# Kernel optimization log

Hardware: AMD Instinct MI355X
Metric: run time of the kernel (lower is better)

The kernel has to match this reference:

```python
import jax, jax.numpy as jnp
import numpy as np

N_NODES = 50000
NEG_SLOPE = 0.2


def _gat_conv(x, src, dst, W, a_src, a_dst, b, num_nodes):
    # W: [H*C, F_in]; a_src/a_dst: [H, C]; b: [H*C]
    H, C = a_src.shape
    xp = (x @ W.T).reshape(num_nodes, H, C)              # [N,H,C]
    alpha_s = jnp.sum(xp * a_src[None], axis=-1)          # [N,H]
    alpha_d = jnp.sum(xp * a_dst[None], axis=-1)          # [N,H]
    e = jax.nn.leaky_relu(alpha_s[src] + alpha_d[dst], NEG_SLOPE)  # [E,H]
    # segment softmax over incoming edges of each dst node (self-loops guarantee non-empty segments)
    m = jax.ops.segment_max(e, dst, num_segments=num_nodes)
    e = jnp.exp(e - m[dst])
    s = jax.ops.segment_sum(e, dst, num_segments=num_nodes)
    alpha = e / s[dst]                                    # [E,H]
    out = jax.ops.segment_sum(alpha[:, :, None] * xp[src], dst, num_segments=num_nodes)  # [N,H,C]
    return out.reshape(num_nodes, H * C) + b


def setup_inputs() -> dict:
    key = jax.random.key(0)
    ks = jax.random.split(key, 12)
    N, E, F_in, HID, H, Z = N_NODES, 800000, 128, 64, 2, 32
    sc = 0.1
    return {
        "features": jax.random.normal(ks[0], (N, F_in), jnp.float32),
        "edges": jax.random.randint(ks[1], (2, E), 0, N, jnp.int32),
        "W1": jax.random.normal(ks[2], (H * HID, F_in), jnp.float32) * sc,
        "a_src1": jax.random.normal(ks[3], (H, HID), jnp.float32) * sc,
        "a_dst1": jax.random.normal(ks[4], (H, HID), jnp.float32) * sc,
        "b1": jnp.zeros((H * HID,), jnp.float32),
        "W_mu": jax.random.normal(ks[5], (Z, H * HID), jnp.float32) * sc,
        "a_src_mu": jax.random.normal(ks[6], (1, Z), jnp.float32) * sc,
        "a_dst_mu": jax.random.normal(ks[7], (1, Z), jnp.float32) * sc,
        "b_mu": jnp.zeros((Z,), jnp.float32),
        "W_std": jax.random.normal(ks[8], (Z, H * HID), jnp.float32) * sc,
        "a_src_std": jax.random.normal(ks[9], (1, Z), jnp.float32) * sc,
        "a_dst_std": jax.random.normal(ks[10], (1, Z), jnp.float32) * sc,
        "b_std": jnp.zeros((Z,), jnp.float32),
    }


def reference(features, edges, W1, a_src1, a_dst1, b1, W_mu, a_src_mu, a_dst_mu, b_mu, W_std, a_src_std, a_dst_std, b_std):
    N = features.shape[0]
    loops = jnp.arange(N, dtype=edges.dtype)
    src = jnp.concatenate([edges[0], loops])  # add self loops (PyG default)
    dst = jnp.concatenate([edges[1], loops])
    h = _gat_conv(features, src, dst, W1, a_src1, a_dst1, b1, N)
    h = jax.nn.relu(h)  # dropout p=0.0 -> identity
    mu = _gat_conv(h, src, dst, W_mu, a_src_mu, a_dst_mu, b_mu, N)
    std = _gat_conv(h, src, dst, W_std, a_src_std, a_dst_std, b_std, N)
    return (mu, std)
```

## Files before the change

### kernel.cpp

```cpp
#include <hip/hip_runtime.h>
#include <math.h>

#define N_NODES 50000
#define N_EDGES 800000
#define ET (N_EDGES + N_NODES)
#define KD 128
#define Z 32
#define SH 7
#define BW 128
#define NBUCK ((N_NODES + BW - 1) / BW)
#define CHUNK 2048
#define NBLKA ((ET + CHUNK - 1) / CHUNK)
#define MTOT (NBUCK * NBLKA)
#define MBS ((MTOT + 1023) / 1024)

typedef __attribute__((ext_vector_type(8))) short bf16x8;
typedef __attribute__((ext_vector_type(4))) float f32x4;

static __device__ __forceinline__ float lrelu(float x){ return x > 0.f ? x : 0.2f*x; }
static __device__ __forceinline__ float bf2f(unsigned int u16){ return __uint_as_float(u16 << 16); }
static __device__ __forceinline__ float lof(unsigned int u){ return __uint_as_float(u << 16); }
static __device__ __forceinline__ float hif(unsigned int u){ return __uint_as_float(u & 0xffff0000u); }
static __device__ __forceinline__ unsigned short f2bf(float f){
  unsigned int x = __float_as_uint(f);
  return (unsigned short)((x + 0x7fffu + ((x >> 16) & 1u)) >> 16);
}

__global__ __launch_bounds__(256) void bhistA_kernel(const int* __restrict__ edges, int* __restrict__ M){
  int k = blockIdx.x, t = threadIdx.x;
  __shared__ int cnt[NBUCK];
  for(int b = t; b < NBUCK; b += 256) cnt[b] = 0;
  __syncthreads();
  int base = k*CHUNK;
  int lim = min(base + CHUNK, ET);
  for(int i = base + t; i < lim; i += 256){
    int d = (i < N_EDGES) ? edges[N_EDGES + i] : (i - N_EDGES);
    atomicAdd(&cnt[d >> SH], 1);
  }
  __syncthreads();
  for(int b = t; b < NBUCK; b += 256) M[b*NBLKA + k] = cnt[b];
}

__global__ __launch_bounds__(256) void scanM1_kernel(const int* __restrict__ M, int* __restrict__ bsumM){
  int b = blockIdx.x, t = threadIdx.x;
  int base = b*1024 + t*4;
  int s = 0;
  #pragma unroll
  for(int i=0;i<4;i++){ int n = base+i; if(n < MTOT) s += M[n]; }
  for(int off=32; off; off>>=1) s += __shfl_xor(s, off);
  __shared__ int ws[4];
  if((t&63)==0) ws[t>>6] = s;
  __syncthreads();
  if(t==0) bsumM[b] = ws[0]+ws[1]+ws[2]+ws[3];
}

__global__ __launch_bounds__(256) void scanM2_kernel(const int* __restrict__ bsumM, int* __restrict__ bpreM){
  __shared__ int sm[256];
  int t = threadIdx.x;
  int v = (t < MBS) ? bsumM[t] : 0;
  sm[t] = v;
  __syncthreads();
  for(int off=1; off<256; off<<=1){
    int u = (t >= off) ? sm[t-off] : 0;
    __syncthreads();
    sm[t] += u;
    __syncthreads();
  }
  if(t < MBS) bpreM[t] = sm[t] - v;
}

__global__ __launch_bounds__(256) void scanM3_kernel(const int* __restrict__ M, const int* __restrict__ bpreM,
                                                     int* __restrict__ Mpos){
  int b = blockIdx.x, t = threadIdx.x;
  int lane = t & 63, wv = t >> 6;
  int base = b*1024 + t*4;
  int d[4]; int s = 0;
  #pragma unroll
  for(int i=0;i<4;i++){ int n = base+i; d[i] = (n < MTOT) ? M[n] : 0; s += d[i]; }
  int v = s;
  for(int off=1; off<64; off<<=1){
    int u = __shfl_up(v, off);
    if(lane >= off) v += u;
  }
  int texcl = v - s;
  __shared__ int wtot[4];
  if(lane == 63) wtot[wv] = v;
  __syncthreads();
  int woff = 0;
  for(int i=0;i<wv;i++) woff += wtot[i];
  int run = bpreM[b] + woff + texcl;
  #pragma unroll
  for(int i=0;i<4;i++){
    int n = base+i;
    if(n < MTOT){ Mpos[n] = run; run += d[i]; }
  }
}

__global__ __launch_bounds__(256) void bplaceA_kernel(const int* __restrict__ edges, const int* __restrict__ Mpos,
                                                      int2* __restrict__ etmp){
  int k = blockIdx.x, t = threadIdx.x;
  __shared__ int cur[NBUCK];
  for(int b = t; b < NBUCK; b += 256) cur[b] = Mpos[b*NBLKA + k];
  __syncthreads();
  int base = k*CHUNK;
  int lim = min(base + CHUNK, ET);
  for(int i = base + t; i < lim; i += 256){
    int s, d;
    if(i < N_EDGES){ s = edges[i]; d = edges[N_EDGES+i]; } else { s = d = i - N_EDGES; }
    int pos = atomicAdd(&cur[d >> SH], 1);
    etmp[pos] = make_int2(s, d);
  }
}

__global__ __launch_bounds__(256) void bfin_kernel(const int* __restrict__ Mpos, const int2* __restrict__ etmp,
                                                   int* __restrict__ rowptr, int2* __restrict__ epair){
  int b = blockIdx.x, t = threadIdx.x;
  __shared__ int cnt[BW];
  __shared__ int pre[BW];
  __shared__ int lcur[BW];
  if(t < BW) cnt[t] = 0;
  __syncthreads();
  int beg = Mpos[b*NBLKA];
  int end = (b+1 < NBUCK) ? Mpos[(b+1)*NBLKA] : ET;
  for(int i = beg + t; i < end; i += 256) atomicAdd(&cnt[etmp[i].y & (BW-1)], 1);
  __syncthreads();
  if(t < BW) pre[t] = cnt[t];
  __syncthreads();
  for(int off=1; off<BW; off<<=1){
    int u = 0;
    if(t < BW && t >= off) u = pre[t-off];
    __syncthreads();
    if(t < BW) pre[t] += u;
    __syncthreads();
  }
  if(t < BW){
    int excl = pre[t] - cnt[t];
    int node = b*BW + t;
    if(node < N_NODES) rowptr[node] = beg + excl;
    lcur[t] = beg + excl;
  }
  if(b == 0 && t == 255) rowptr[N_NODES] = ET;
  __syncthreads();
  for(int i = beg + t; i < end; i += 256){
    int2 e = etmp[i];
    int pos = atomicAdd(&lcur[e.y & (BW-1)], 1);
    epair[pos] = e;
  }
}

__global__ __launch_bounds__(256) void wconv_kernel(const float* __restrict__ W1,
                                                    const float* __restrict__ Wmu, const float* __restrict__ Wst,
                                                    unsigned short* __restrict__ Wb1, unsigned short* __restrict__ Wb2){
  int i = blockIdx.x*256 + threadIdx.x;
  if(i < 128*KD) Wb1[i] = f2bf(W1[i]);
  if(i < 64*KD) Wb2[i] = f2bf(i < 32*KD ? Wmu[i] : Wst[i - 32*KD]);
}

__global__ __launch_bounds__(256) void mmt1_kernel(const float* __restrict__ X,
                                                   const unsigned short* __restrict__ Wb,
                                                   const float* __restrict__ asv, const float* __restrict__ adv,
                                                   unsigned short* __restrict__ outb,
                                                   float* __restrict__ as1, float* __restrict__ ad1){
  constexpr int OC = 128, CT = 8;
  int t = threadIdx.x;
  int w = t >> 6, L = t & 63;
  int col = L & 15, quad = L >> 4;
  int row0 = blockIdx.x*64 + w*16;
  int rA = row0 + col;
  if(rA >= N_NODES) rA = N_NODES-1;

  f32x4 acc[CT];
  #pragma unroll
  for(int ct=0;ct<CT;ct++) acc[ct] = (f32x4){0.f,0.f,0.f,0.f};

  #pragma unroll
  for(int kc=0;kc<4;kc++){
    int k0 = kc*32 + quad*8;
    const float* Xf = X + (size_t)rA*KD + k0;
    float4 p = *(const float4*)Xf;
    float4 q = *(const float4*)(Xf + 4);
    bf16x8 a;
    a[0] = (short)f2bf(p.x); a[1] = (short)f2bf(p.y);
    a[2] = (short)f2bf(p.z); a[3] = (short)f2bf(p.w);
    a[4] = (short)f2bf(q.x); a[5] = (short)f2bf(q.y);
    a[6] = (short)f2bf(q.z); a[7] = (short)f2bf(q.w);
    #pragma unroll
    for(int ct=0;ct<CT;ct++){
      bf16x8 b = *(const bf16x8*)(Wb + (size_t)(ct*16 + col)*KD + k0);
      acc[ct] = __builtin_amdgcn_mfma_f32_16x16x32_bf16(a, b, acc[ct], 0, 0, 0);
    }
  }

  float av[CT], dv[CT];
  #pragma unroll
  for(int ct=0;ct<CT;ct++){ av[ct] = asv[ct*16 + col]; dv[ct] = adv[ct*16 + col]; }

  #pragma unroll
  for(int r=0;r<4;r++){
    int row = row0 + quad*4 + r;
    #pragma unroll
    for(int ct=0;ct<CT;ct++)
      if(row < N_NODES) outb[(size_t)row*OC + ct*16 + col] = f2bf(acc[ct][r]);
    float s0 = acc[0][r]*av[0] + acc[1][r]*av[1] + acc[2][r]*av[2] + acc[3][r]*av[3];
    float s1 = acc[4][r]*av[4] + acc[5][r]*av[5] + acc[6][r]*av[6] + acc[7][r]*av[7];
    float d0 = acc[0][r]*dv[0] + acc[1][r]*dv[1] + acc[2][r]*dv[2] + acc[3][r]*dv[3];
    float d1 = acc[4][r]*dv[4] + acc[5][r]*dv[5] + acc[6][r]*dv[6] + acc[7][r]*dv[7];
    #pragma unroll
    for(int off=1; off<16; off<<=1){
      s0 += __shfl_xor(s0, off); s1 += __shfl_xor(s1, off);
      d0 += __shfl_xor(d0, off); d1 += __shfl_xor(d1, off);
    }
    if(col == 0 && row < N_NODES){
      as1[row*2] = s0; as1[row*2+1] = s1;
      ad1[row*2] = d0; ad1[row*2+1] = d1;
    }
  }
}

__global__ __launch_bounds__(256) void mmt2_kernel(const unsigned short* __restrict__ Xb,
                                                   const unsigned short* __restrict__ Wb,
                                                   const float* __restrict__ asmu, const float* __restrict__ admu,
                                                   const float* __restrict__ asst, const float* __restrict__ adst,
                                                   unsigned short* __restrict__ outb,
                                                   float* __restrict__ as2, float* __restrict__ ad2){
  constexpr int OC = 64, CT = 4;
  int t = threadIdx.x;
  int w = t >> 6, L = t & 63;
  int col = L & 15, quad = L >> 4;
  int row0 = blockIdx.x*64 + w*16;
  int rA = row0 + col;
  if(rA >= N_NODES) rA = N_NODES-1;

  f32x4 acc[CT];
  #pragma unroll
  for(int ct=0;ct<CT;ct++) acc[ct] = (f32x4){0.f,0.f,0.f,0.f};

  #pragma unroll
  for(int kc=0;kc<4;kc++){
    int k0 = kc*32 + quad*8;
    bf16x8 a = *(const bf16x8*)(Xb + (size_t)rA*KD + k0);
    #pragma unroll
    for(int ct=0;ct<CT;ct++){
      bf16x8 b = *(const bf16x8*)(Wb + (size_t)(ct*16 + col)*KD + k0);
      acc[ct] = __builtin_amdgcn_mfma_f32_16x16x32_bf16(a, b, acc[ct], 0, 0, 0);
    }
  }

  float av[CT], dv[CT];
  #pragma unroll
  for(int ct=0;ct<CT;ct++){
    av[ct] = (ct < 2) ? asmu[ct*16 + col] : asst[(ct-2)*16 + col];
    dv[ct] = (ct < 2) ? admu[ct*16 + col] : adst[(ct-2)*16 + col];
  }

  #pragma unroll
  for(int r=0;r<4;r++){
    int row = row0 + quad*4 + r;
    #pragma unroll
    for(int ct=0;ct<CT;ct++)
      if(row < N_NODES) outb[(size_t)row*OC + ct*16 + col] = f2bf(acc[ct][r]);
    float smu = acc[0][r]*av[0] + acc[1][r]*av[1];
    float sst = acc[2][r]*av[2] + acc[3][r]*av[3];
    float dmu = acc[0][r]*dv[0] + acc[1][r]*dv[1];
    float dst = acc[2][r]*dv[2] + acc[3][r]*dv[3];
    #pragma unroll
    for(int off=1; off<16; off<<=1){
      smu += __shfl_xor(smu, off); sst += __shfl_xor(sst, off);
      dmu += __shfl_xor(dmu, off); dst += __shfl_xor(dst, off);
    }
    if(col == 0 && row < N_NODES){
      as2[row*2] = smu; as2[row*2+1] = sst;
      ad2[row*2] = dmu; ad2[row*2+1] = dst;
    }
  }
}

__global__ __launch_bounds__(256) void wcalc_kernel(const int2* __restrict__ epair,
                                                    const float* __restrict__ asv, const float* __restrict__ adv,
                                                    float2* __restrict__ wbuf){
  int i = blockIdx.x*256 + threadIdx.x;
  if(i >= ET) return;
  int2 e = epair[i];
  float2 a = ((const float2*)asv)[e.x];
  float2 b = ((const float2*)adv)[e.y];
  float2 w;
  w.x = __expf(lrelu(a.x + b.x));
  w.y = __expf(lrelu(a.y + b.y));
  wbuf[i] = w;
}

__global__ __launch_bounds__(256) void agg1_kernel(const int* __restrict__ rowptr, const int2* __restrict__ epair,
                                                   const float2* __restrict__ wbuf, const uint2* __restrict__ xb,
                                                   const float* __restrict__ b1, uint2* __restrict__ hb){
  int node = blockIdx.x*4 + (threadIdx.x>>6);
  int l = threadIdx.x & 63;
  if(node >= N_NODES) return;
  int half = l >> 5, c = l & 31;
  int beg = rowptr[node], end = rowptr[node+1];
  int n = end - beg;
  float a0=0.f, a1=0.f, a2=0.f, a3=0.f, s0=0.f, s1=0.f;
  int npair = n >> 1;
  int mainp = npair & ~7;

#define G1(j) int e##j = epair[base + 2*j].x; float2 w##j = wbuf[base + 2*j];
#define U1(j) uint2 u##j = xb[(size_t)e##j*32 + c];
#define C1(j) { s0 += w##j.x; s1 += w##j.y; \
                float vv = (c < 16) ? w##j.x : w##j.y; \
                a0 += vv*lof(u##j.x); a1 += vv*hif(u##j.x); \
                a2 += vv*lof(u##j.y); a3 += vv*hif(u##j.y); }

  for(int pq = 0; pq < mainp; pq += 8){
    int base = beg + 2*pq + half;
    G1(0) G1(1) G1(2) G1(3) G1(4) G1(5) G1(6) G1(7)
    U1(0) U1(1) U1(2) U1(3) U1(4) U1(5) U1(6) U1(7)
    C1(0) C1(1) C1(2) C1(3) C1(4) C1(5) C1(6) C1(7)
  }
  for(int pq = mainp; pq < npair; pq++){
    int base = beg + 2*pq + half;
    G1(0) U1(0) C1(0)
  }
  if((n & 1) && half == 0){
    int idx = beg + n - 1;
    int e = epair[idx].x;
    float2 w = wbuf[idx];
    uint2 u = xb[(size_t)e*32 + c];
    s0 += w.x; s1 += w.y;
    float vv = (c < 16) ? w.x : w.y;
    a0 += vv*lof(u.x); a1 += vv*hif(u.x);
    a2 += vv*lof(u.y); a3 += vv*hif(u.y);
  }
#undef G1
#undef U1
#undef C1
  s0 += __shfl_xor(s0, 32); s1 += __shfl_xor(s1, 32);
  a0 += __shfl_xor(a0, 32); a1 += __shfl_xor(a1, 32);
  a2 += __shfl_xor(a2, 32); a3 += __shfl_xor(a3, 32);
  float sd = (c < 16) ? s0 : s1;
  float4 bb = *(const float4*)(b1 + 4*c);
  float r0 = fmaxf(a0/sd + bb.x, 0.f);
  float r1 = fmaxf(a1/sd + bb.y, 0.f);
  float r2 = fmaxf(a2/sd + bb.z, 0.f);
  float r3 = fmaxf(a3/sd + bb.w, 0.f);
  if(half == 0){
    uint2 o;
    o.x = (unsigned)f2bf(r0) | ((unsigned)f2bf(r1) << 16);
    o.y = (unsigned)f2bf(r2) | ((unsigned)f2bf(r3) << 16);
    hb[(size_t)node*32 + c] = o;
  }
}

__global__ __launch_bounds__(256) void agg2_kernel(const int* __restrict__ rowptr, const int2* __restrict__ epair,
                                                   const float2* __restrict__ wbuf, const uint2* __restrict__ xb2,
                                                   const float* __restrict__ bmu, const float* __restrict__ bst,
                                                   float* __restrict__ out){
  int node = blockIdx.x*4 + (threadIdx.x>>6);
  int l = threadIdx.x & 63;
  if(node >= N_NODES) return;
  int g = l >> 4, c = l & 15;
  int beg = rowptr[node], end = rowptr[node+1];
  int n = end - beg;
  float a0=0.f, a1=0.f, a2=0.f, a3=0.f, smu=0.f, sst=0.f;
  int nquad = n >> 2;
  int mainq = nquad & ~3;

#define G2(j) int e##j = epair[base + 4*j].x; float2 w##j = wbuf[base + 4*j];
#define U2(j) uint2 u##j = xb2[(size_t)e##j*16 + c];
#define C2(j) { smu += w##j.x; sst += w##j.y; \
                float vv = (c < 8) ? w##j.x : w##j.y; \
                a0 += vv*lof(u##j.x); a1 += vv*hif(u##j.x); \
                a2 += vv*lof(u##j.y); a3 += vv*hif(u##j.y); }

  for(int qq = 0; qq < mainq; qq += 4){
    int base = beg + 4*qq + g;
    G2(0) G2(1) G2(2) G2(3)
    U2(0) U2(1) U2(2) U2(3)
    C2(0) C2(1) C2(2) C2(3)
  }
  for(int qq = mainq; qq < nquad; qq++){
    int base = beg + 4*qq + g;
    G2(0) U2(0) C2(0)
  }
  int tail = n & 3;
  if(g < tail){
    int idx = beg + 4*nquad + g;
    int e = epair[idx].x;
    float2 w = wbuf[idx];
    uint2 u = xb2[(size_t)e*16 + c];
    smu += w.x; sst += w.y;
    float vv = (c < 8) ? w.x : w.y;
    a0 += vv*lof(u.x); a1 += vv*hif(u.x);
    a2 += vv*lof(u.y); a3 += vv*hif(u.y);
  }
#undef G2
#undef U2
#undef C2
  #pragma unroll
  for(int off = 16; off < 64; off <<= 1){
    smu += __shfl_xor(smu, off); sst += __shfl_xor(sst, off);
    a0 += __shfl_xor(a0, off); a1 += __shfl_xor(a1, off);
    a2 += __shfl_xor(a2, off); a3 += __shfl_xor(a3, off);
  }
  float sd = (c < 8) ? smu : sst;
  float4 bb = (c < 8) ? *(const float4*)(bmu + 4*c) : *(const float4*)(bst + 4*(c-8));
  float4 r;
  r.x = a0/sd + bb.x;
  r.y = a1/sd + bb.y;
  r.z = a2/sd + bb.z;
  r.w = a3/sd + bb.w;
  if(g == 0){
    float* dst = (c < 8) ? (out + (size_t)node*Z + 4*c)
                         : (out + (size_t)N_NODES*Z + (size_t)node*Z + 4*(c-8));
    *(float4*)dst = r;
  }
}

extern "C" void kernel_launch(void* const* d_in, const int* in_sizes, int n_in,
                              void* d_out, int out_size, void* d_ws, size_t ws_size,
                              hipStream_t stream){
  const float* x    = (const float*)d_in[0];
  const int*   edges= (const int*)d_in[1];
  const float* W1   = (const float*)d_in[2];
  const float* as1v = (const float*)d_in[3];
  const float* ad1v = (const float*)d_in[4];
  const float* b1   = (const float*)d_in[5];
  const float* Wmu  = (const float*)d_in[6];
  const float* asmu = (const float*)d_in[7];
  const float* admu = (const float*)d_in[8];
  const float* bmu  = (const float*)d_in[9];
  const float* Wst  = (const float*)d_in[10];
  const float* asst = (const float*)d_in[11];
  const float* adst = (const float*)d_in[12];
  const float* bst  = (const float*)d_in[13];
  float* out = (float*)d_out;

  char* p = (char*)d_ws;
  auto alloc = [&](size_t bytes)->char*{ char* r = p; p += (bytes + 255) & ~size_t(255); return r; };
  int*   M      = (int*)  alloc((size_t)MTOT*4);
  int*   Mpos   = (int*)  alloc((size_t)MTOT*4);
  int*   bsumM  = (int*)  alloc((size_t)MBS*4);
  int*   bpreM  = (int*)  alloc((size_t)MBS*4);
  int2*  etmp   = (int2*) alloc((size_t)ET*8);
  int2*  epair  = (int2*) alloc((size_t)ET*8);
  int*   rowptr = (int*)  alloc((size_t)(N_NODES+1)*4);
  unsigned short* Wb1 = (unsigned short*)alloc((size_t)128*KD*2);
  unsigned short* Wb2 = (unsigned short*)alloc((size_t)64*KD*2);
  unsigned short* xpb1 = (unsigned short*)alloc((size_t)N_NODES*128*2);
  float* as1    = (float*)alloc((size_t)N_NODES*2*4);
  float* ad1    = (float*)alloc((size_t)N_NODES*2*4);
  unsigned short* hb = (unsigned short*)alloc((size_t)N_NODES*128*2);
  float2* wbuf  = (float2*)alloc((size_t)ET*8);
  float* as2    = (float*)alloc((size_t)N_NODES*2*4);
  float* ad2    = (float*)alloc((size_t)N_NODES*2*4);
  unsigned short* xpb2 = xpb1;

  bhistA_kernel  <<<NBLKA, 256, 0, stream>>>(edges, M);
  scanM1_kernel  <<<MBS, 256, 0, stream>>>(M, bsumM);
  scanM2_kernel  <<<1, 256, 0, stream>>>(bsumM, bpreM);
  scanM3_kernel  <<<MBS, 256, 0, stream>>>(M, bpreM, Mpos);
  bplaceA_kernel <<<NBLKA, 256, 0, stream>>>(edges, Mpos, etmp);
  bfin_kernel    <<<NBUCK, 256, 0, stream>>>(Mpos, etmp, rowptr, epair);

  wconv_kernel   <<<(128*KD + 255)/256, 256, 0, stream>>>(W1, Wmu, Wst, Wb1, Wb2);

  mmt1_kernel <<<(N_NODES+63)/64, 256, 0, stream>>>(x, Wb1, as1v, ad1v, xpb1, as1, ad1);
  wcalc_kernel<<<(ET+255)/256, 256, 0, stream>>>(epair, as1, ad1, wbuf);
  agg1_kernel <<<(N_NODES+3)/4, 256, 0, stream>>>(rowptr, epair, wbuf, (const uint2*)xpb1, b1, (uint2*)hb);

  mmt2_kernel <<<(N_NODES+63)/64, 256, 0, stream>>>(hb, Wb2, asmu, admu, asst, adst, xpb1, as2, ad2);
  wcalc_kernel<<<(ET+255)/256, 256, 0, stream>>>(epair, as2, ad2, wbuf);
  agg2_kernel <<<(N_NODES+3)/4, 256, 0, stream>>>(rowptr, epair, wbuf, (const uint2*)xpb2, bmu, bst, out);
}
```

Baseline: 250.5 us.

## Fuse edge-weight computation into aggregation kernels and store only source indices

Removes the separate wcalc kernels and the per-edge weight buffer. Each aggregation now computes exp(leaky_relu(alpha_s[src]+alpha_d[node])) inline, which works because the destination is fixed per node. The CSR edge array now holds 4-byte source ids instead of int2 pairs. agg1 is also remapped so that 64 lanes each handle one 32-bit element per edge instead of two half-waves handling two edges each, and the bucketing chunk size is doubled. In exchange, every lane recomputes the exp and issues an extra gather of alpha_s.

```diff
diff --git a/kernel.cpp b/kernel.cpp
--- a/kernel.cpp
+++ b/kernel.cpp
@@ -9,7 +9,7 @@
 #define SH 7
 #define BW 128
 #define NBUCK ((N_NODES + BW - 1) / BW)
-#define CHUNK 2048
+#define CHUNK 4096
 #define NBLKA ((ET + CHUNK - 1) / CHUNK)
 #define MTOT (NBUCK * NBLKA)
 #define MBS ((MTOT + 1023) / 1024)
@@ -113,7 +113,7 @@
 }
 
 __global__ __launch_bounds__(256) void bfin_kernel(const int* __restrict__ Mpos, const int2* __restrict__ etmp,
-                                                   int* __restrict__ rowptr, int2* __restrict__ epair){
+                                                   int* __restrict__ rowptr, int* __restrict__ esrc){
   int b = blockIdx.x, t = threadIdx.x;
   __shared__ int cnt[BW];
   __shared__ int pre[BW];
@@ -144,7 +144,7 @@
   for(int i = beg + t; i < end; i += 256){
     int2 e = etmp[i];
     int pos = atomicAdd(&lcur[e.y & (BW-1)], 1);
-    epair[pos] = e;
+    esrc[pos] = e.x;
   }
 }
 
@@ -275,82 +275,53 @@
   }
 }
 
-__global__ __launch_bounds__(256) void wcalc_kernel(const int2* __restrict__ epair,
-                                                    const float* __restrict__ asv, const float* __restrict__ adv,
-                                                    float2* __restrict__ wbuf){
-  int i = blockIdx.x*256 + threadIdx.x;
-  if(i >= ET) return;
-  int2 e = epair[i];
-  float2 a = ((const float2*)asv)[e.x];
-  float2 b = ((const float2*)adv)[e.y];
-  float2 w;
-  w.x = __expf(lrelu(a.x + b.x));
-  w.y = __expf(lrelu(a.y + b.y));
-  wbuf[i] = w;
-}
-
-__global__ __launch_bounds__(256) void agg1_kernel(const int* __restrict__ rowptr, const int2* __restrict__ epair,
-                                                   const float2* __restrict__ wbuf, const uint2* __restrict__ xb,
-                                                   const float* __restrict__ b1, uint2* __restrict__ hb){
+__global__ __launch_bounds__(256) void agg1_kernel(const int* __restrict__ rowptr, const int* __restrict__ esrc,
+                                                   const float* __restrict__ as1, const float* __restrict__ ad1,
+                                                   const unsigned int* __restrict__ xb,
+                                                   const float* __restrict__ b1, unsigned int* __restrict__ hb){
   int node = blockIdx.x*4 + (threadIdx.x>>6);
   int l = threadIdx.x & 63;
   if(node >= N_NODES) return;
-  int half = l >> 5, c = l & 31;
   int beg = rowptr[node], end = rowptr[node+1];
+  const float2* asp = (const float2*)as1;
+  float2 adn = ((const float2*)ad1)[node];
+  float accx = 0.f, accy = 0.f, s0 = 0.f, s1 = 0.f;
   int n = end - beg;
-  float a0=0.f, a1=0.f, a2=0.f, a3=0.f, s0=0.f, s1=0.f;
-  int npair = n >> 1;
-  int mainp = npair & ~7;
-
-#define G1(j) int e##j = epair[base + 2*j].x; float2 w##j = wbuf[base + 2*j];
-#define U1(j) uint2 u##j = xb[(size_t)e##j*32 + c];
-#define C1(j) { s0 += w##j.x; s1 += w##j.y; \
-                float vv = (c < 16) ? w##j.x : w##j.y; \
-                a0 += vv*lof(u##j.x); a1 += vv*hif(u##j.x); \
-                a2 += vv*lof(u##j.y); a3 += vv*hif(u##j.y); }
-
-  for(int pq = 0; pq < mainp; pq += 8){
-    int base = beg + 2*pq + half;
-    G1(0) G1(1) G1(2) G1(3) G1(4) G1(5) G1(6) G1(7)
-    U1(0) U1(1) U1(2) U1(3) U1(4) U1(5) U1(6) U1(7)
-    C1(0) C1(1) C1(2) C1(3) C1(4) C1(5) C1(6) C1(7)
-  }
-  for(int pq = mainp; pq < npair; pq++){
-    int base = beg + 2*pq + half;
-    G1(0) U1(0) C1(0)
-  }
-  if((n & 1) && half == 0){
-    int idx = beg + n - 1;
-    int e = epair[idx].x;
-    float2 w = wbuf[idx];
-    uint2 u = xb[(size_t)e*32 + c];
-    s0 += w.x; s1 += w.y;
-    float vv = (c < 16) ? w.x : w.y;
-    a0 += vv*lof(u.x); a1 += vv*hif(u.x);
-    a2 += vv*lof(u.y); a3 += vv*hif(u.y);
-  }
-#undef G1
-#undef U1
-#undef C1
-  s0 += __shfl_xor(s0, 32); s1 += __shfl_xor(s1, 32);
-  a0 += __shfl_xor(a0, 32); a1 += __shfl_xor(a1, 32);
-  a2 += __shfl_xor(a2, 32); a3 += __shfl_xor(a3, 32);
-  float sd = (c < 16) ? s0 : s1;
-  float4 bb = *(const float4*)(b1 + 4*c);
-  float r0 = fmaxf(a0/sd + bb.x, 0.f);
-  float r1 = fmaxf(a1/sd + bb.y, 0.f);
-  float r2 = fmaxf(a2/sd + bb.z, 0.f);
-  float r3 = fmaxf(a3/sd + bb.w, 0.f);
-  if(half == 0){
-    uint2 o;
-    o.x = (unsigned)f2bf(r0) | ((unsigned)f2bf(r1) << 16);
-    o.y = (unsigned)f2bf(r2) | ((unsigned)f2bf(r3) << 16);
-    hb[(size_t)node*32 + c] = o;
-  }
-}
-
-__global__ __launch_bounds__(256) void agg2_kernel(const int* __restrict__ rowptr, const int2* __restrict__ epair,
-                                                   const float2* __restrict__ wbuf, const uint2* __restrict__ xb2,
+  int nq = n & ~7;
+
+#define F1_E(j)  int e##j = esrc[i+j];
+#define F1_A(j)  float2 a##j = asp[e##j];
+#define F1_U(j)  unsigned int u##j = xb[(size_t)e##j*64 + l];
+#define F1_C(j)  { float wx = __expf(lrelu(a##j.x + adn.x)); \
+                   float wy = __expf(lrelu(a##j.y + adn.y)); \
+                   s0 += wx; s1 += wy; \
+                   float vv = (l < 32) ? wx : wy; \
+                   accx += vv * lof(u##j); accy += vv * hif(u##j); }
+
+  for(int i = beg; i < beg + nq; i += 8){
+    F1_E(0) F1_E(1) F1_E(2) F1_E(3) F1_E(4) F1_E(5) F1_E(6) F1_E(7)
+    F1_A(0) F1_A(1) F1_A(2) F1_A(3) F1_A(4) F1_A(5) F1_A(6) F1_A(7)
+    F1_U(0) F1_U(1) F1_U(2) F1_U(3) F1_U(4) F1_U(5) F1_U(6) F1_U(7)
+    F1_C(0) F1_C(1) F1_C(2) F1_C(3) F1_C(4) F1_C(5) F1_C(6) F1_C(7)
+  }
+  for(int i = beg + nq; i < end; i++){
+    F1_E(0) F1_A(0) F1_U(0) F1_C(0)
+  }
+#undef F1_E
+#undef F1_A
+#undef F1_U
+#undef F1_C
+  float sd = (l < 32) ? s0 : s1;
+  float2 bb = ((const float2*)b1)[l];
+  float rx = fmaxf(accx/sd + bb.x, 0.f);
+  float ry = fmaxf(accy/sd + bb.y, 0.f);
+  unsigned int hp = (unsigned int)f2bf(rx) | ((unsigned int)f2bf(ry) << 16);
+  hb[(size_t)node*64 + l] = hp;
+}
+
+__global__ __launch_bounds__(256) void agg2_kernel(const int* __restrict__ rowptr, const int* __restrict__ esrc,
+                                                   const float* __restrict__ as2, const float* __restrict__ ad2,
+                                                   const uint2* __restrict__ xb2,
                                                    const float* __restrict__ bmu, const float* __restrict__ bst,
                                                    float* __restrict__ out){
   int node = blockIdx.x*4 + (threadIdx.x>>6);
@@ -358,15 +329,19 @@
   if(node >= N_NODES) return;
   int g = l >> 4, c = l & 15;
   int beg = rowptr[node], end = rowptr[node+1];
+  const float2* asp = (const float2*)as2;
+  float2 adn = ((const float2*)ad2)[node];
   int n = end - beg;
   float a0=0.f, a1=0.f, a2=0.f, a3=0.f, smu=0.f, sst=0.f;
   int nquad = n >> 2;
   int mainq = nquad & ~3;
 
-#define G2(j) int e##j = epair[base + 4*j].x; float2 w##j = wbuf[base + 4*j];
+#define G2(j) int e##j = esrc[base + 4*j]; float2 aa##j = asp[e##j];
 #define U2(j) uint2 u##j = xb2[(size_t)e##j*16 + c];
-#define C2(j) { smu += w##j.x; sst += w##j.y; \
-                float vv = (c < 8) ? w##j.x : w##j.y; \
+#define C2(j) { float wx = __expf(lrelu(aa##j.x + adn.x)); \
+                float wy = __expf(lrelu(aa##j.y + adn.y)); \
+                smu += wx; sst += wy; \
+                float vv = (c < 8) ? wx : wy; \
                 a0 += vv*lof(u##j.x); a1 += vv*hif(u##j.x); \
                 a2 += vv*lof(u##j.y); a3 += vv*hif(u##j.y); }
 
@@ -383,11 +358,13 @@
   int tail = n & 3;
   if(g < tail){
     int idx = beg + 4*nquad + g;
-    int e = epair[idx].x;
-    float2 w = wbuf[idx];
+    int e = esrc[idx];
+    float2 aa = asp[e];
     uint2 u = xb2[(size_t)e*16 + c];
-    smu += w.x; sst += w.y;
-    float vv = (c < 8) ? w.x : w.y;
+    float wx = __expf(lrelu(aa.x + adn.x));
+    float wy = __expf(lrelu(aa.y + adn.y));
+    smu += wx; sst += wy;
+    float vv = (c < 8) ? wx : wy;
     a0 += vv*lof(u.x); a1 += vv*hif(u.x);
     a2 += vv*lof(u.y); a3 += vv*hif(u.y);
   }
@@ -440,7 +417,7 @@
   int*   bsumM  = (int*)  alloc((size_t)MBS*4);
   int*   bpreM  = (int*)  alloc((size_t)MBS*4);
   int2*  etmp   = (int2*) alloc((size_t)ET*8);
-  int2*  epair  = (int2*) alloc((size_t)ET*8);
+  int*   esrc   = (int*)  alloc((size_t)ET*4);
   int*   rowptr = (int*)  alloc((size_t)(N_NODES+1)*4);
   unsigned short* Wb1 = (unsigned short*)alloc((size_t)128*KD*2);
   unsigned short* Wb2 = (unsigned short*)alloc((size_t)64*KD*2);
@@ -448,7 +425,6 @@
   float* as1    = (float*)alloc((size_t)N_NODES*2*4);
   float* ad1    = (float*)alloc((size_t)N_NODES*2*4);
   unsigned short* hb = (unsigned short*)alloc((size_t)N_NODES*128*2);
-  float2* wbuf  = (float2*)alloc((size_t)ET*8);
   float* as2    = (float*)alloc((size_t)N_NODES*2*4);
   float* ad2    = (float*)alloc((size_t)N_NODES*2*4);
   unsigned short* xpb2 = xpb1;
@@ -458,15 +434,13 @@
   scanM2_kernel  <<<1, 256, 0, stream>>>(bsumM, bpreM);
   scanM3_kernel  <<<MBS, 256, 0, stream>>>(M, bpreM, Mpos);
   bplaceA_kernel <<<NBLKA, 256, 0, stream>>>(edges, Mpos, etmp);
-  bfin_kernel    <<<NBUCK, 256, 0, stream>>>(Mpos, etmp, rowptr, epair);
+  bfin_kernel    <<<NBUCK, 256, 0, stream>>>(Mpos, etmp, rowptr, esrc);
 
   wconv_kernel   <<<(128*KD + 255)/256, 256, 0, stream>>>(W1, Wmu, Wst, Wb1, Wb2);
 
   mmt1_kernel <<<(N_NODES+63)/64, 256, 0, stream>>>(x, Wb1, as1v, ad1v, xpb1, as1, ad1);
-  wcalc_kernel<<<(ET+255)/256, 256, 0, stream>>>(epair, as1, ad1, wbuf);
-  agg1_kernel <<<(N_NODES+3)/4, 256, 0, stream>>>(rowptr, epair, wbuf, (const uint2*)xpb1, b1, (uint2*)hb);
+  agg1_kernel <<<(N_NODES+3)/4, 256, 0, stream>>>(rowptr, esrc, as1, ad1, (const unsigned int*)xpb1, b1, (unsigned int*)hb);
 
   mmt2_kernel <<<(N_NODES+63)/64, 256, 0, stream>>>(hb, Wb2, asmu, admu, asst, adst, xpb1, as2, ad2);
-  wcalc_kernel<<<(ET+255)/256, 256, 0, stream>>>(epair, as2, ad2, wbuf);
-  agg2_kernel <<<(N_NODES+3)/4, 256, 0, stream>>>(rowptr, epair, wbuf, (const uint2*)xpb2, bmu, bst, out);
-}
+  agg2_kernel <<<(N_NODES+3)/4, 256, 0, stream>>>(rowptr, esrc, as2, ad2, (const uint2*)xpb2, bmu, bst, out);
+}
```

New measurement: 249.4 us. No clear change (-0.5%).
